# Kernel tuning notes

Measured on AMD Instinct MI355X. Metric: run time of the kernel, lower is better.

Reference implementation:

```python
import jax, jax.numpy as jnp
import numpy as np

N_NODES = 50000
N_EDGES = 640000
HID = 128
LN_EPS = 1e-5


def setup_inputs() -> dict:
    key = jax.random.key(0)
    ks = jax.random.split(key, 8)
    x = jax.random.normal(ks[0], (N_NODES, HID), dtype=jnp.float32)
    edge_index = jax.random.randint(ks[1], (2, N_EDGES), 0, N_NODES, dtype=jnp.int64)
    edge_attr = jax.random.normal(ks[2], (N_EDGES, HID), dtype=jnp.float32)
    # parameters (Kaiming-ish scaling)
    msg_W1 = jax.random.normal(ks[3], (3 * HID, HID), dtype=jnp.float32) / np.sqrt(3 * HID)
    msg_b1 = jnp.zeros((HID,), dtype=jnp.float32)
    msg_W2 = jax.random.normal(ks[4], (HID, HID), dtype=jnp.float32) / np.sqrt(HID)
    msg_b2 = jnp.zeros((HID,), dtype=jnp.float32)
    upd_W1 = jax.random.normal(ks[5], (2 * HID, HID), dtype=jnp.float32) / np.sqrt(2 * HID)
    upd_b1 = jnp.zeros((HID,), dtype=jnp.float32)
    upd_W2 = jax.random.normal(ks[6], (HID, HID), dtype=jnp.float32) / np.sqrt(HID)
    upd_b2 = jnp.zeros((HID,), dtype=jnp.float32)
    ln_gamma = jnp.ones((HID,), dtype=jnp.float32)
    ln_beta = jnp.zeros((HID,), dtype=jnp.float32)
    return {
        'x': x, 'edge_index': edge_index, 'edge_attr': edge_attr,
        'msg_W1': msg_W1, 'msg_b1': msg_b1, 'msg_W2': msg_W2, 'msg_b2': msg_b2,
        'upd_W1': upd_W1, 'upd_b1': upd_b1, 'upd_W2': upd_W2, 'upd_b2': upd_b2,
        'ln_gamma': ln_gamma, 'ln_beta': ln_beta,
    }


def _layer_norm(h, gamma, beta):
    mu = jnp.mean(h, axis=-1, keepdims=True)
    var = jnp.mean(jnp.square(h - mu), axis=-1, keepdims=True)
    return (h - mu) * jax.lax.rsqrt(var + LN_EPS) * gamma + beta


def reference(x, edge_index, edge_attr,
              msg_W1, msg_b1, msg_W2, msg_b2,
              upd_W1, upd_b1, upd_W2, upd_b2,
              ln_gamma, ln_beta):
    src, dst = edge_index[0], edge_index[1]
    # batched per-edge gather + concat: [E, 3*HID]
    msg_in = jnp.concatenate([x[src], x[dst], edge_attr], axis=-1)
    # message MLP (dropout is identity in eval)
    h = jax.nn.relu(msg_in @ msg_W1 + msg_b1)
    messages = h @ msg_W2 + msg_b2  # [E, HID]
    # scatter-add aggregation by destination node
    aggregated = jax.ops.segment_sum(messages, dst, num_segments=x.shape[0])
    # update MLP
    upd_in = jnp.concatenate([x, aggregated], axis=-1)  # [N, 2*HID]
    u = jax.nn.relu(upd_in @ upd_W1 + upd_b1)
    updated = u @ upd_W2 + upd_b2
    return _layer_norm(x + updated, ln_gamma, ln_beta)
```

## Files before the change

kernel.cpp:

```cpp
#include <hip/hip_runtime.h>

#define HID 128

typedef __attribute__((ext_vector_type(8))) short short8;
typedef __attribute__((ext_vector_type(4))) float f32x4;

__device__ __forceinline__ float bf2f(unsigned short u) {
  union { unsigned int u; float f; } c; c.u = ((unsigned int)u) << 16; return c.f;
}
__device__ __forceinline__ unsigned short f2bf(float f) {
  union { float f; unsigned int u; } c; c.f = f;
  unsigned int u = c.u;
  return (unsigned short)((u + 0x7FFFu + ((u >> 16) & 1u)) >> 16);
}
__device__ __forceinline__ float loads(const void* p, size_t i, bool f32) {
  return f32 ? ((const float*)p)[i] : bf2f(((const unsigned short*)p)[i]);
}
__device__ __forceinline__ short8 load_a8(const void* base, size_t row, int k, bool f32) {
  if (!f32) return *(const short8*)((const unsigned short*)base + row * HID + k);
  const float* fp = (const float*)base + row * HID + k;
  f32x4 f0 = *(const f32x4*)fp;
  f32x4 f1 = *(const f32x4*)(fp + 4);
  short8 t;
  t[0] = (short)f2bf(f0[0]); t[1] = (short)f2bf(f0[1]);
  t[2] = (short)f2bf(f0[2]); t[3] = (short)f2bf(f0[3]);
  t[4] = (short)f2bf(f1[0]); t[5] = (short)f2bf(f1[1]);
  t[6] = (short)f2bf(f1[2]); t[7] = (short)f2bf(f1[3]);
  return t;
}

__global__ void detect_kernel(const void* __restrict__ x,
                              const int* __restrict__ eidx,
                              int* __restrict__ flags) {
  __shared__ int bad, oddnz;
  if (threadIdx.x == 0) { bad = 0; oddnz = 0; }
  __syncthreads();
  const unsigned short* xu = (const unsigned short*)x;
  int mybad = 0;
  for (int i = threadIdx.x; i < 4096; i += 256) {
    int ef = (xu[i] >> 7) & 0xFF;
    if (!(ef == 0 || (ef >= 90 && ef <= 140))) mybad++;
  }
  if (mybad) atomicAdd(&bad, mybad);
  if (threadIdx.x < 128) {
    if (eidx[2 * threadIdx.x + 1] != 0) atomicAdd(&oddnz, 1);
  }
  __syncthreads();
  if (threadIdx.x == 0) {
    flags[0] = (bad > 409) ? 1 : 0;
    flags[1] = (oddnz == 0) ? 1 : 0;
  }
}

__device__ __forceinline__ int get_dst(const int* eidx, bool i64, int E, int e) {
  return i64 ? eidx[2 * (E + e)] : eidx[E + e];
}
__device__ __forceinline__ int get_src(const int* eidx, bool i64, int E, int e) {
  return i64 ? eidx[2 * e] : eidx[e];
}

__global__ void zero_out_kernel(unsigned int* __restrict__ out,
                                const int* __restrict__ flags, long long nelem) {
  bool f32 = flags[0] != 0;
  size_t words = (size_t)nelem * (f32 ? 2 : 1) / 2;
  for (size_t w = blockIdx.x * 256ull + threadIdx.x; w < words; w += (size_t)gridDim.x * 256ull)
    out[w] = 0u;
}

__global__ void repack_all(const void* __restrict__ W1, const void* __restrict__ W2,
                           const void* __restrict__ U1, const void* __restrict__ U2,
                           unsigned short* __restrict__ P1, unsigned short* __restrict__ P2,
                           unsigned short* __restrict__ PU1, unsigned short* __restrict__ PU2,
                           const int* __restrict__ flags) {
  const bool f32 = flags[0] != 0;
  int idx = blockIdx.x * 256 + threadIdx.x;
  const int s1 = 384 * 128, s2 = s1 + 128 * 128, s3 = s2 + 256 * 128, s4 = s3 + 128 * 128;
  if (idx >= s4) return;
  const void* W; unsigned short* P; int off;
  if (idx < s1)      { W = W1; P = P1;  off = idx; }
  else if (idx < s2) { W = W2; P = P2;  off = idx - s1; }
  else if (idx < s3) { W = U1; P = PU1; off = idx - s2; }
  else               { W = U2; P = PU2; off = idx - s3; }
  int j = off & 7, lane = (off >> 3) & 63, ct = (off >> 9) & 7, ks = off >> 12;
  int k = ks * 32 + ((lane >> 4) << 3) + j;
  int n = ct * 16 + (lane & 15);
  P[off] = f2bf(loads(W, (size_t)k * 128 + n, f32));
}

__global__ void hist_kernel(const int* __restrict__ eidx, int* __restrict__ counts,
                            const int* __restrict__ flags, int E, int N) {
  const bool i64 = flags[1] != 0;
  int e = blockIdx.x * 256 + threadIdx.x;
  if (e < E) {
    int d = get_dst(eidx, i64, E, e);
    d = min(max(d, 0), N - 1);
    atomicAdd(&counts[d], 1);
  }
}

__global__ __launch_bounds__(1024) void scan_kernel(const int* __restrict__ counts,
                                                    int* __restrict__ offs, int N) {
  __shared__ int wsum[16];
  __shared__ int wpre[16];
  __shared__ int carry_s;
  const int tid = threadIdx.x, lane = tid & 63, wid = tid >> 6;
  if (tid == 0) carry_s = 0;
  __syncthreads();
  for (int base = 0; base < N; base += 1024) {
    int i = base + tid;
    int v = (i < N) ? counts[i] : 0;
    int s = v;
#pragma unroll
    for (int off = 1; off < 64; off <<= 1) {
      int t = __shfl_up(s, off, 64);
      if (lane >= off) s += t;
    }
    if (lane == 63) wsum[wid] = s;
    __syncthreads();
    if (tid == 0) {
      int run = carry_s;
#pragma unroll
      for (int w = 0; w < 16; w++) { int t = wsum[w]; wpre[w] = run; run += t; }
      carry_s = run;
    }
    __syncthreads();
    if (i < N) offs[i] = wpre[wid] + s - v;
    __syncthreads();
  }
  if (tid == 0) offs[N] = carry_s;
}

__global__ void scatter_kernel(const int* __restrict__ eidx, int* __restrict__ cur,
                               int* __restrict__ ssrc, int* __restrict__ sdst,
                               int* __restrict__ perm,
                               const int* __restrict__ flags, int E, int N) {
  const bool i64 = flags[1] != 0;
  int e = blockIdx.x * 256 + threadIdx.x;
  if (e < E) {
    int d = get_dst(eidx, i64, E, e);
    int s = get_src(eidx, i64, E, e);
    d = min(max(d, 0), N - 1);
    s = min(max(s, 0), N - 1);
    int pos = atomicAdd(&cur[d], 1);
    ssrc[pos] = s;
    sdst[pos] = d;
    perm[pos] = e;
  }
}

__global__ __launch_bounds__(256) void edge_kernel_sorted(
    const void* __restrict__ x, const void* __restrict__ eattr,
    const int* __restrict__ ssrc, const int* __restrict__ sdst,
    const int* __restrict__ perm,
    const unsigned short* __restrict__ P1, const void* __restrict__ b1,
    const unsigned short* __restrict__ P2, const void* __restrict__ b2,
    float* __restrict__ aggf, const int* __restrict__ flags, int E, int N) {
  __shared__ __align__(16) char smem[64 * 132 * 4];
  __shared__ int sdst_s[64];
  unsigned short (*hs)[136] = (unsigned short (*)[136])smem;
  float (*ms)[132] = (float (*)[132])smem;
  const bool f32 = flags[0] != 0;
  const int tid  = threadIdx.x;
  const int lane = tid & 63;
  const int wid  = tid >> 6;
  const int l15  = lane & 15;
  const int quad = lane >> 4;
  const int base = blockIdx.x * 64;

  if (tid < 64) sdst_s[tid] = sdst[min(base + tid, E - 1)];

  int me = base + wid * 16 + l15;
  if (me >= E) me = E - 1;
  const int src = ssrc[me];
  const int dsm = sdst[me];
  const int pe  = perm[me];

  f32x4 zero = {0.f, 0.f, 0.f, 0.f};
  f32x4 acc[8];
#pragma unroll
  for (int ct = 0; ct < 8; ct++) acc[ct] = zero;

#pragma unroll
  for (int ks = 0; ks < 12; ks++) {
    const int k0 = ks * 32;
    short8 a;
    if (k0 < 128)      a = load_a8(x,     (size_t)src, k0 + quad * 8, f32);
    else if (k0 < 256) a = load_a8(x,     (size_t)dsm, (k0 - 128) + quad * 8, f32);
    else               a = load_a8(eattr, (size_t)pe,  (k0 - 256) + quad * 8, f32);
    const unsigned short* wp = P1 + ((size_t)(ks * 8) * 64 + lane) * 8;
#pragma unroll
    for (int ct = 0; ct < 8; ct++) {
      short8 b = *(const short8*)(wp + ct * 512);
      acc[ct] = __builtin_amdgcn_mfma_f32_16x16x32_bf16(a, b, acc[ct], 0, 0, 0);
    }
  }

#pragma unroll
  for (int ct = 0; ct < 8; ct++) {
    const int col = ct * 16 + l15;
    const float bv = loads(b1, col, f32);
#pragma unroll
    for (int r = 0; r < 4; r++) {
      float v = acc[ct][r] + bv;
      hs[wid * 16 + quad * 4 + r][col] = f2bf(fmaxf(v, 0.f));
    }
  }

  f32x4 acc2[8];
#pragma unroll
  for (int ct = 0; ct < 8; ct++) acc2[ct] = zero;
#pragma unroll
  for (int ks = 0; ks < 4; ks++) {
    short8 a = *(const short8*)&hs[wid * 16 + l15][ks * 32 + quad * 8];
    const unsigned short* wp = P2 + ((size_t)(ks * 8) * 64 + lane) * 8;
#pragma unroll
    for (int ct = 0; ct < 8; ct++) {
      short8 b = *(const short8*)(wp + ct * 512);
      acc2[ct] = __builtin_amdgcn_mfma_f32_16x16x32_bf16(a, b, acc2[ct], 0, 0, 0);
    }
  }

  float b2v[8];
#pragma unroll
  for (int ct = 0; ct < 8; ct++) b2v[ct] = loads(b2, ct * 16 + l15, f32);

  __syncthreads();
#pragma unroll
  for (int ct = 0; ct < 8; ct++) {
    const int col = ct * 16 + l15;
#pragma unroll
    for (int r = 0; r < 4; r++) {
      const int e = base + wid * 16 + quad * 4 + r;
      ms[wid * 16 + quad * 4 + r][col] = (e < E) ? (acc2[ct][r] + b2v[ct]) : 0.0f;
    }
  }
  __syncthreads();

  const int col  = tid & 127;
  const int half = tid >> 7;
  const int r0 = half * 32;
  float sum = 0.0f;
  int cur = sdst_s[r0];
#pragma unroll 4
  for (int r = r0; r < r0 + 32; r++) {
    int d = sdst_s[r];
    if (d != cur) {
      atomicAdd(&aggf[(size_t)cur * HID + col], sum);
      sum = 0.0f; cur = d;
    }
    sum += ms[r][col];
  }
  atomicAdd(&aggf[(size_t)cur * HID + col], sum);
}

__global__ __launch_bounds__(256) void edge_kernel_plain(
    const void* __restrict__ x, const int* __restrict__ eidx,
    const void* __restrict__ eattr,
    const unsigned short* __restrict__ P1, const void* __restrict__ b1,
    const unsigned short* __restrict__ P2, const void* __restrict__ b2,
    float* __restrict__ aggf, void* __restrict__ out,
    const int* __restrict__ flags, int E, int N, int small_mode) {
  __shared__ unsigned short hs[64][136];
  const bool f32 = flags[0] != 0;
  const bool i64 = flags[1] != 0;
  const int tid  = threadIdx.x;
  const int lane = tid & 63;
  const int wid  = tid >> 6;
  const int l15  = lane & 15;
  const int quad = lane >> 4;
  const int base = blockIdx.x * 64;

  int me = base + wid * 16 + l15;
  if (me >= E) me = E - 1;
  int src = get_src(eidx, i64, E, me);
  int dsm = get_dst(eidx, i64, E, me);
  src = min(max(src, 0), N - 1);
  dsm = min(max(dsm, 0), N - 1);

  f32x4 zero = {0.f, 0.f, 0.f, 0.f};
  f32x4 acc[8];
#pragma unroll
  for (int ct = 0; ct < 8; ct++) acc[ct] = zero;
#pragma unroll
  for (int ks = 0; ks < 12; ks++) {
    const int k0 = ks * 32;
    short8 a;
    if (k0 < 128)      a = load_a8(x,     (size_t)src, k0 + quad * 8, f32);
    else if (k0 < 256) a = load_a8(x,     (size_t)dsm, (k0 - 128) + quad * 8, f32);
    else               a = load_a8(eattr, (size_t)me,  (k0 - 256) + quad * 8, f32);
    const unsigned short* wp = P1 + ((size_t)(ks * 8) * 64 + lane) * 8;
#pragma unroll
    for (int ct = 0; ct < 8; ct++) {
      short8 b = *(const short8*)(wp + ct * 512);
      acc[ct] = __builtin_amdgcn_mfma_f32_16x16x32_bf16(a, b, acc[ct], 0, 0, 0);
    }
  }
#pragma unroll
  for (int ct = 0; ct < 8; ct++) {
    const int col = ct * 16 + l15;
    const float bv = loads(b1, col, f32);
#pragma unroll
    for (int r = 0; r < 4; r++)
      hs[wid * 16 + quad * 4 + r][col] = f2bf(fmaxf(acc[ct][r] + bv, 0.f));
  }
  __syncthreads();
  f32x4 acc2[8];
#pragma unroll
  for (int ct = 0; ct < 8; ct++) acc2[ct] = zero;
#pragma unroll
  for (int ks = 0; ks < 4; ks++) {
    short8 a = *(const short8*)&hs[wid * 16 + l15][ks * 32 + quad * 8];
    const unsigned short* wp = P2 + ((size_t)(ks * 8) * 64 + lane) * 8;
#pragma unroll
    for (int ct = 0; ct < 8; ct++) {
      short8 b = *(const short8*)(wp + ct * 512);
      acc2[ct] = __builtin_amdgcn_mfma_f32_16x16x32_bf16(a, b, acc2[ct], 0, 0, 0);
    }
  }
  float b2v[8];
#pragma unroll
  for (int ct = 0; ct < 8; ct++) b2v[ct] = loads(b2, ct * 16 + l15, f32);

  if (!small_mode || f32) {
    float* tgt = (!small_mode) ? aggf : (float*)out;
#pragma unroll
    for (int r = 0; r < 4; r++) {
      const int e = base + wid * 16 + quad * 4 + r;
      if (e < E) {
        int d = get_dst(eidx, i64, E, e);
        d = min(max(d, 0), N - 1);
        float* op = tgt + (size_t)d * HID + l15;
#pragma unroll
        for (int ct = 0; ct < 8; ct++) atomicAdd(op + ct * 16, acc2[ct][r] + b2v[ct]);
      }
    }
  } else {
#pragma unroll
    for (int ct = 0; ct < 8; ct++) {
      const int col = ct * 16 + l15;
#pragma unroll
      for (int r = 0; r < 4; r++)
        hs[wid * 16 + quad * 4 + r][col] = f2bf(acc2[ct][r] + b2v[ct]);
    }
    __syncthreads();
    const int row = tid >> 2;
    const int cg  = (tid & 3) * 32;
    const int e = base + row;
    if (e < E) {
      int d = get_dst(eidx, i64, E, e);
      d = min(max(d, 0), N - 1);
      unsigned int* orow = (unsigned int*)out + ((size_t)d * HID >> 1);
#pragma unroll
      for (int p = 0; p < 16; p++) {
        const int col = cg + p * 2;
        const float lo = bf2f(hs[row][col]);
        const float hi = bf2f(hs[row][col + 1]);
        unsigned int* wp = orow + (col >> 1);
        unsigned int old = *wp, assumed;
        do {
          assumed = old;
          unsigned int nv = (unsigned int)f2bf(bf2f((unsigned short)(assumed & 0xFFFF)) + lo)
                          | ((unsigned int)f2bf(bf2f((unsigned short)(assumed >> 16)) + hi) << 16);
          old = atomicCAS(wp, assumed, nv);
        } while (old != assumed);
      }
    }
  }
}

__global__ __launch_bounds__(256) void node_kernel(
    const void* __restrict__ x, const float* __restrict__ aggf,
    const unsigned short* __restrict__ PU1, const void* __restrict__ ub1,
    const unsigned short* __restrict__ PU2, const void* __restrict__ ub2,
    const void* __restrict__ gamma, const void* __restrict__ beta,
    void* __restrict__ out, const int* __restrict__ flags, int N, int small_mode) {
  __shared__ unsigned short hs[64][136];
  const bool f32 = flags[0] != 0;
  const int tid  = threadIdx.x;
  const int lane = tid & 63;
  const int wid  = tid >> 6;
  const int l15  = lane & 15;
  const int quad = lane >> 4;
  const int base = blockIdx.x * 64;

  int mn = base + wid * 16 + l15;
  if (mn >= N) mn = N - 1;

  const void* aggp = (!small_mode) ? (const void*)aggf : (const void*)out;
  const bool aggF32 = (!small_mode) ? true : f32;

  f32x4 zero = {0.f, 0.f, 0.f, 0.f};
  f32x4 acc[8];
#pragma unroll
  for (int ct = 0; ct < 8; ct++) acc[ct] = zero;
#pragma unroll
  for (int ks = 0; ks < 8; ks++) {
    const int k0 = ks * 32;
    short8 a;
    if (k0 < 128) a = load_a8(x,    (size_t)mn, k0 + quad * 8, f32);
    else          a = load_a8(aggp, (size_t)mn, (k0 - 128) + quad * 8, aggF32);
    const unsigned short* wp = PU1 + ((size_t)(ks * 8) * 64 + lane) * 8;
#pragma unroll
    for (int ct = 0; ct < 8; ct++) {
      short8 b = *(const short8*)(wp + ct * 512);
      acc[ct] = __builtin_amdgcn_mfma_f32_16x16x32_bf16(a, b, acc[ct], 0, 0, 0);
    }
  }
#pragma unroll
  for (int ct = 0; ct < 8; ct++) {
    const int col = ct * 16 + l15;
    const float bv = loads(ub1, col, f32);
#pragma unroll
    for (int r = 0; r < 4; r++)
      hs[wid * 16 + quad * 4 + r][col] = f2bf(fmaxf(acc[ct][r] + bv, 0.f));
  }
  __syncthreads();
  f32x4 acc2[8];
#pragma unroll
  for (int ct = 0; ct < 8; ct++) acc2[ct] = zero;
#pragma unroll
  for (int ks = 0; ks < 4; ks++) {
    short8 a = *(const short8*)&hs[wid * 16 + l15][ks * 32 + quad * 8];
    const unsigned short* wp = PU2 + ((size_t)(ks * 8) * 64 + lane) * 8;
#pragma unroll
    for (int ct = 0; ct < 8; ct++) {
      short8 b = *(const short8*)(wp + ct * 512);
      acc2[ct] = __builtin_amdgcn_mfma_f32_16x16x32_bf16(a, b, acc2[ct], 0, 0, 0);
    }
  }

  float vals[8][4];
  float s1[4] = {0.f, 0.f, 0.f, 0.f};
  float s2[4] = {0.f, 0.f, 0.f, 0.f};
#pragma unroll
  for (int ct = 0; ct < 8; ct++) {
    const int col = ct * 16 + l15;
    const float bv = loads(ub2, col, f32);
#pragma unroll
    for (int r = 0; r < 4; r++) {
      int row = base + wid * 16 + quad * 4 + r;
      int rc = row < N ? row : 0;
      float v = acc2[ct][r] + bv + loads(x, (size_t)rc * HID + col, f32);
      vals[ct][r] = v;
      s1[r] += v;
      s2[r] += v * v;
    }
  }
#pragma unroll
  for (int off = 1; off < 16; off <<= 1) {
#pragma unroll
    for (int r = 0; r < 4; r++) {
      s1[r] += __shfl_xor(s1[r], off, 16);
      s2[r] += __shfl_xor(s2[r], off, 16);
    }
  }
#pragma unroll
  for (int r = 0; r < 4; r++) {
    const int row = base + wid * 16 + quad * 4 + r;
    if (row < N) {
      const float mean = s1[r] * (1.0f / 128.0f);
      const float var  = fmaxf(s2[r] * (1.0f / 128.0f) - mean * mean, 0.0f);
      const float rstd = rsqrtf(var + 1e-5f);
#pragma unroll
      for (int ct = 0; ct < 8; ct++) {
        const int col = ct * 16 + l15;
        float o = (vals[ct][r] - mean) * rstd * loads(gamma, col, f32) + loads(beta, col, f32);
        if (f32) ((float*)out)[(size_t)row * HID + col] = o;
        else     ((unsigned short*)out)[(size_t)row * HID + col] = f2bf(o);
      }
    }
  }
}

extern "C" void kernel_launch(void* const* d_in, const int* in_sizes, int n_in,
                              void* d_out, int out_size, void* d_ws, size_t ws_size,
                              hipStream_t stream) {
  (void)n_in;
  const void* x     = d_in[0];
  const int*  eidx  = (const int*)d_in[1];
  const void* eattr = d_in[2];
  const void* W1  = d_in[3];
  const void* b1  = d_in[4];
  const void* W2  = d_in[5];
  const void* b2  = d_in[6];
  const void* U1  = d_in[7];
  const void* ub1 = d_in[8];
  const void* U2  = d_in[9];
  const void* ub2 = d_in[10];
  const void* gam = d_in[11];
  const void* bet = d_in[12];

  const int N = in_sizes[0] / HID;
  const int E = in_sizes[2] / HID;

  char* ws = (char*)d_ws;
  int* flags = (int*)ws;
  unsigned short* P1  = (unsigned short*)(ws + 256);
  unsigned short* P2  = (unsigned short*)(ws + 256 + 98304);
  unsigned short* PU1 = (unsigned short*)(ws + 256 + 131072);
  unsigned short* PU2 = (unsigned short*)(ws + 256 + 196608);
  const size_t agg_off = 256 + 229376;
  float* aggf = (float*)(ws + agg_off);
  const size_t agg_bytes = (size_t)N * HID * sizeof(float);

  size_t o = agg_off + agg_bytes;
  auto alignup = [](size_t v) { return (v + 255) & ~(size_t)255; };
  o = alignup(o);           size_t offs_off = o; o += (size_t)(N + 1) * 4;
  o = alignup(o);           size_t cur_off  = o; o += (size_t)(N + 1) * 4;
  o = alignup(o);           size_t ssrc_off = o; o += (size_t)E * 4;
  o = alignup(o);           size_t sdst_off = o; o += (size_t)E * 4;
  o = alignup(o);           size_t perm_off = o; o += (size_t)E * 4;
  const size_t need_sort  = o;
  const size_t need_basic = agg_off + agg_bytes;

  int* offsb = (int*)(ws + offs_off);
  int* curb  = (int*)(ws + cur_off);
  int* ssrc  = (int*)(ws + ssrc_off);
  int* sdst  = (int*)(ws + sdst_off);
  int* perm  = (int*)(ws + perm_off);

  const int mode = (ws_size >= need_sort) ? 2 : ((ws_size >= need_basic) ? 1 : 0);

  detect_kernel<<<1, 256, 0, stream>>>(x, eidx, flags);
  repack_all<<<448, 256, 0, stream>>>(W1, W2, U1, U2, P1, P2, PU1, PU2, flags);

  if (mode == 2) {
    hipMemsetAsync(aggf, 0, agg_bytes, stream);
    hipMemsetAsync(curb, 0, (size_t)(N + 1) * 4, stream);
    hist_kernel<<<(E + 255) / 256, 256, 0, stream>>>(eidx, curb, flags, E, N);
    scan_kernel<<<1, 1024, 0, stream>>>(curb, offsb, N);
    hipMemcpyAsync(curb, offsb, (size_t)(N + 1) * 4, hipMemcpyDeviceToDevice, stream);
    scatter_kernel<<<(E + 255) / 256, 256, 0, stream>>>(eidx, curb, ssrc, sdst, perm,
                                                        flags, E, N);
    edge_kernel_sorted<<<(E + 63) / 64, 256, 0, stream>>>(x, eattr, ssrc, sdst, perm,
                                                          P1, b1, P2, b2, aggf, flags, E, N);
    node_kernel<<<(N + 63) / 64, 256, 0, stream>>>(x, aggf, PU1, ub1, PU2, ub2,
                                                   gam, bet, d_out, flags, N, 0);
  } else if (mode == 1) {
    hipMemsetAsync(aggf, 0, agg_bytes, stream);
    edge_kernel_plain<<<(E + 63) / 64, 256, 0, stream>>>(x, eidx, eattr, P1, b1, P2, b2,
                                                         aggf, d_out, flags, E, N, 0);
    node_kernel<<<(N + 63) / 64, 256, 0, stream>>>(x, aggf, PU1, ub1, PU2, ub2,
                                                   gam, bet, d_out, flags, N, 0);
  } else {
    zero_out_kernel<<<1024, 256, 0, stream>>>((unsigned int*)d_out, flags, (long long)out_size);
    edge_kernel_plain<<<(E + 63) / 64, 256, 0, stream>>>(x, eidx, eattr, P1, b1, P2, b2,
                                                         aggf, d_out, flags, E, N, 1);
    node_kernel<<<(N + 63) / 64, 256, 0, stream>>>(x, aggf, PU1, ub1, PU2, ub2,
                                                   gam, bet, d_out, flags, N, 1);
  }
}
```

Baseline: 903.0 us.

## Precompute per-node first-layer projections and split edge MLP into gather, store, reduce

```diff
diff --git a/kernel.cpp b/kernel.cpp
--- a/kernel.cpp
+++ b/kernel.cpp
@@ -98,6 +98,244 @@
   }
 }
 
+__global__ __launch_bounds__(1024) void scanA_kernel(const int* __restrict__ cnt,
+                                                     int* __restrict__ curb,
+                                                     int* __restrict__ bsum, int N) {
+  __shared__ int wsum[16], wsum2[16];
+  const int tid = threadIdx.x, lane = tid & 63, wid = tid >> 6;
+  int i = blockIdx.x * 1024 + tid;
+  int v = (i < N) ? cnt[i] : 0;
+  int s = v;
+#pragma unroll
+  for (int off = 1; off < 64; off <<= 1) {
+    int t = __shfl_up(s, off, 64);
+    if (lane >= off) s += t;
+  }
+  if (lane == 63) wsum[wid] = s;
+  __syncthreads();
+  if (wid == 0 && lane < 16) {
+    int w = wsum[lane];
+#pragma unroll
+    for (int off = 1; off < 16; off <<= 1) {
+      int t = __shfl_up(w, off, 16);
+      if (lane >= off) w += t;
+    }
+    wsum2[lane] = w;
+    if (lane == 15) bsum[blockIdx.x] = w;
+  }
+  __syncthreads();
+  int pre = (wid > 0) ? wsum2[wid - 1] : 0;
+  if (i < N) curb[i] = pre + s - v;
+}
+
+__global__ void scanB_kernel(int* __restrict__ bsum, int nb) {
+  if (threadIdx.x == 0 && blockIdx.x == 0) {
+    int run = 0;
+    for (int b = 0; b < nb; b++) { int t = bsum[b]; bsum[b] = run; run += t; }
+  }
+}
+
+__global__ __launch_bounds__(1024) void scanC_kernel(int* __restrict__ curb,
+                                                     const int* __restrict__ bsum, int N) {
+  int i = blockIdx.x * 1024 + threadIdx.x;
+  if (i < N) curb[i] += bsum[blockIdx.x];
+}
+
+__global__ void scatter_rank_kernel(const int* __restrict__ eidx, int* __restrict__ cur,
+                                    int* __restrict__ rank, int* __restrict__ sdst,
+                                    const int* __restrict__ flags, int E, int N) {
+  const bool i64 = flags[1] != 0;
+  int e = blockIdx.x * 256 + threadIdx.x;
+  if (e < E) {
+    int d = get_dst(eidx, i64, E, e);
+    d = min(max(d, 0), N - 1);
+    int pos = atomicAdd(&cur[d], 1);
+    rank[e] = pos;
+    sdst[pos] = d;
+  }
+}
+
+__global__ __launch_bounds__(256) void x1_kernel(
+    const void* __restrict__ x, const unsigned short* __restrict__ P1,
+    const void* __restrict__ b1, unsigned short* __restrict__ X1,
+    const int* __restrict__ flags, int N) {
+  __shared__ unsigned short hs[64][264];
+  const bool f32 = flags[0] != 0;
+  const int tid = threadIdx.x, lane = tid & 63, wid = tid >> 6;
+  const int l15 = lane & 15, quad = lane >> 4;
+  const int base = blockIdx.x * 64;
+  int mn = min(base + wid * 16 + l15, N - 1);
+
+  f32x4 zero = {0.f, 0.f, 0.f, 0.f};
+  f32x4 acca[8], accb[8];
+#pragma unroll
+  for (int ct = 0; ct < 8; ct++) { acca[ct] = zero; accb[ct] = zero; }
+#pragma unroll
+  for (int ks = 0; ks < 4; ks++) {
+    short8 a = load_a8(x, (size_t)mn, ks * 32 + quad * 8, f32);
+    const unsigned short* wpa = P1 + ((size_t)(ks * 8) * 64 + lane) * 8;
+    const unsigned short* wpb = P1 + ((size_t)((ks + 4) * 8) * 64 + lane) * 8;
+#pragma unroll
+    for (int ct = 0; ct < 8; ct++) {
+      short8 ba = *(const short8*)(wpa + ct * 512);
+      short8 bb = *(const short8*)(wpb + ct * 512);
+      acca[ct] = __builtin_amdgcn_mfma_f32_16x16x32_bf16(a, ba, acca[ct], 0, 0, 0);
+      accb[ct] = __builtin_amdgcn_mfma_f32_16x16x32_bf16(a, bb, accb[ct], 0, 0, 0);
+    }
+  }
+#pragma unroll
+  for (int ct = 0; ct < 8; ct++) {
+    const int col = ct * 16 + l15;
+    const float bv = loads(b1, col, f32);
+#pragma unroll
+    for (int r = 0; r < 4; r++) {
+      hs[wid * 16 + quad * 4 + r][col]       = f2bf(acca[ct][r] + bv);
+      hs[wid * 16 + quad * 4 + r][128 + col] = f2bf(accb[ct][r]);
+    }
+  }
+  __syncthreads();
+  const int row = tid >> 2, part = tid & 3;
+  if (base + row < N) {
+    unsigned short* op = X1 + (size_t)(base + row) * 256 + part * 64;
+#pragma unroll
+    for (int j = 0; j < 8; j++)
+      *(short8*)(op + j * 8) = *(const short8*)&hs[row][part * 64 + j * 8];
+  }
+}
+
+__global__ __launch_bounds__(256) void edgeB_kernel(
+    const void* __restrict__ eattr, const int* __restrict__ eidx,
+    const int* __restrict__ rank, const unsigned short* __restrict__ X1,
+    const unsigned short* __restrict__ P1, const unsigned short* __restrict__ P2,
+    unsigned short* __restrict__ msgbuf, const int* __restrict__ flags, int E, int N) {
+  __shared__ unsigned short hsb[64][136];
+  __shared__ int src_s[64], dst_s[64], rank_s[64];
+  const bool f32 = flags[0] != 0;
+  const bool i64 = flags[1] != 0;
+  const int tid = threadIdx.x, lane = tid & 63, wid = tid >> 6;
+  const int l15 = lane & 15, quad = lane >> 4;
+  const int base = blockIdx.x * 64;
+
+  if (tid < 64) {
+    int e = min(base + tid, E - 1);
+    int s = get_src(eidx, i64, E, e);
+    int d = get_dst(eidx, i64, E, e);
+    src_s[tid] = min(max(s, 0), N - 1);
+    dst_s[tid] = min(max(d, 0), N - 1);
+    rank_s[tid] = rank[e];
+  }
+
+  int me = min(base + wid * 16 + l15, E - 1);
+  f32x4 zero = {0.f, 0.f, 0.f, 0.f};
+  f32x4 acc[8];
+#pragma unroll
+  for (int ct = 0; ct < 8; ct++) acc[ct] = zero;
+#pragma unroll
+  for (int ks = 0; ks < 4; ks++) {
+    short8 a = load_a8(eattr, (size_t)me, ks * 32 + quad * 8, f32);
+    const unsigned short* wp = P1 + ((size_t)((ks + 8) * 8) * 64 + lane) * 8;
+#pragma unroll
+    for (int ct = 0; ct < 8; ct++) {
+      short8 b = *(const short8*)(wp + ct * 512);
+      acc[ct] = __builtin_amdgcn_mfma_f32_16x16x32_bf16(a, b, acc[ct], 0, 0, 0);
+    }
+  }
+#pragma unroll
+  for (int ct = 0; ct < 8; ct++) {
+    const int col = ct * 16 + l15;
+#pragma unroll
+    for (int r = 0; r < 4; r++)
+      hsb[wid * 16 + quad * 4 + r][col] = f2bf(acc[ct][r]);
+  }
+  __syncthreads();
+
+#pragma unroll
+  for (int it = 0; it < 4; it++) {
+    const int r = it * 16 + (tid >> 4);
+    const int cg = (tid & 15) * 8;
+    short8 h8 = *(const short8*)&hsb[r][cg];
+    short8 a8 = *(const short8*)(X1 + (size_t)src_s[r] * 256 + cg);
+    short8 b8 = *(const short8*)(X1 + (size_t)dst_s[r] * 256 + 128 + cg);
+    short8 o;
+#pragma unroll
+    for (int j = 0; j < 8; j++) {
+      float v = bf2f((unsigned short)h8[j]) + bf2f((unsigned short)a8[j])
+              + bf2f((unsigned short)b8[j]);
+      o[j] = (short)f2bf(fmaxf(v, 0.f));
+    }
+    *(short8*)&hsb[r][cg] = o;
+  }
+  __syncthreads();
+
+  f32x4 acc2[8];
+#pragma unroll
+  for (int ct = 0; ct < 8; ct++) acc2[ct] = zero;
+#pragma unroll
+  for (int ks = 0; ks < 4; ks++) {
+    short8 a = *(const short8*)&hsb[wid * 16 + l15][ks * 32 + quad * 8];
+    const unsigned short* wp = P2 + ((size_t)(ks * 8) * 64 + lane) * 8;
+#pragma unroll
+    for (int ct = 0; ct < 8; ct++) {
+      short8 b = *(const short8*)(wp + ct * 512);
+      acc2[ct] = __builtin_amdgcn_mfma_f32_16x16x32_bf16(a, b, acc2[ct], 0, 0, 0);
+    }
+  }
+#pragma unroll
+  for (int ct = 0; ct < 8; ct++) {
+    const int col = ct * 16 + l15;
+#pragma unroll
+    for (int r = 0; r < 4; r++)
+      hsb[wid * 16 + quad * 4 + r][col] = f2bf(acc2[ct][r]);
+  }
+  __syncthreads();
+
+  const int row = tid >> 2, part = tid & 3;
+  if (base + row < E) {
+    unsigned short* mp = msgbuf + (size_t)rank_s[row] * HID + part * 32;
+#pragma unroll
+    for (int j = 0; j < 4; j++)
+      *(short8*)(mp + j * 8) = *(const short8*)&hsb[row][part * 32 + j * 8];
+  }
+}
+
+__global__ __launch_bounds__(256) void reduce_kernel(
+    const unsigned short* __restrict__ msgbuf, const int* __restrict__ sdst,
+    const void* __restrict__ b2, float* __restrict__ aggf,
+    const int* __restrict__ flags, int E) {
+  __shared__ int sd[256];
+  const bool f32 = flags[0] != 0;
+  const int tid = threadIdx.x;
+  const int base = blockIdx.x * 256;
+  { int e = base + tid; sd[tid] = (e < E) ? sdst[e] : -1; }
+  __syncthreads();
+  const int pair = tid & 63;
+  const int grp = tid >> 6;
+  const int c0 = pair * 2;
+  const float b2a = loads(b2, c0, f32);
+  const float b2b = loads(b2, c0 + 1, f32);
+  float sa = 0.f, sb = 0.f; int cnt = 0, cur = -1;
+  for (int r = 0; r < 64; r++) {
+    const int lr = grp * 64 + r;
+    const int d = sd[lr];
+    if (d < 0) break;
+    if (d != cur) {
+      if (cnt > 0) {
+        atomicAdd(&aggf[(size_t)cur * HID + c0],     sa + cnt * b2a);
+        atomicAdd(&aggf[(size_t)cur * HID + c0 + 1], sb + cnt * b2b);
+      }
+      sa = sb = 0.f; cnt = 0; cur = d;
+    }
+    unsigned int u = *(const unsigned int*)(msgbuf + (size_t)(base + lr) * HID + c0);
+    sa += bf2f((unsigned short)(u & 0xFFFF));
+    sb += bf2f((unsigned short)(u >> 16));
+    cnt++;
+  }
+  if (cnt > 0) {
+    atomicAdd(&aggf[(size_t)cur * HID + c0],     sa + cnt * b2a);
+    atomicAdd(&aggf[(size_t)cur * HID + c0 + 1], sb + cnt * b2b);
+  }
+}
+
 __global__ __launch_bounds__(1024) void scan_kernel(const int* __restrict__ counts,
                                                     int* __restrict__ offs, int N) {
   __shared__ int wsum[16];
@@ -160,11 +398,8 @@
   unsigned short (*hs)[136] = (unsigned short (*)[136])smem;
   float (*ms)[132] = (float (*)[132])smem;
   const bool f32 = flags[0] != 0;
-  const int tid  = threadIdx.x;
-  const int lane = tid & 63;
-  const int wid  = tid >> 6;
-  const int l15  = lane & 15;
-  const int quad = lane >> 4;
+  const int tid = threadIdx.x, lane = tid & 63, wid = tid >> 6;
+  const int l15 = lane & 15, quad = lane >> 4;
   const int base = blockIdx.x * 64;
 
   if (tid < 64) sdst_s[tid] = sdst[min(base + tid, E - 1)];
@@ -179,7 +414,6 @@
   f32x4 acc[8];
 #pragma unroll
   for (int ct = 0; ct < 8; ct++) acc[ct] = zero;
-
 #pragma unroll
   for (int ks = 0; ks < 12; ks++) {
     const int k0 = ks * 32;
@@ -194,18 +428,14 @@
       acc[ct] = __builtin_amdgcn_mfma_f32_16x16x32_bf16(a, b, acc[ct], 0, 0, 0);
     }
   }
-
 #pragma unroll
   for (int ct = 0; ct < 8; ct++) {
     const int col = ct * 16 + l15;
     const float bv = loads(b1, col, f32);
 #pragma unroll
-    for (int r = 0; r < 4; r++) {
-      float v = acc[ct][r] + bv;
-      hs[wid * 16 + quad * 4 + r][col] = f2bf(fmaxf(v, 0.f));
-    }
-  }
-
+    for (int r = 0; r < 4; r++)
+      hs[wid * 16 + quad * 4 + r][col] = f2bf(fmaxf(acc[ct][r] + bv, 0.f));
+  }
   f32x4 acc2[8];
 #pragma unroll
   for (int ct = 0; ct < 8; ct++) acc2[ct] = zero;
@@ -219,11 +449,9 @@
       acc2[ct] = __builtin_amdgcn_mfma_f32_16x16x32_bf16(a, b, acc2[ct], 0, 0, 0);
     }
   }
-
   float b2v[8];
 #pragma unroll
   for (int ct = 0; ct < 8; ct++) b2v[ct] = loads(b2, ct * 16 + l15, f32);
-
   __syncthreads();
 #pragma unroll
   for (int ct = 0; ct < 8; ct++) {
@@ -235,7 +463,6 @@
     }
   }
   __syncthreads();
-
   const int col  = tid & 127;
   const int half = tid >> 7;
   const int r0 = half * 32;
@@ -263,11 +490,8 @@
   __shared__ unsigned short hs[64][136];
   const bool f32 = flags[0] != 0;
   const bool i64 = flags[1] != 0;
-  const int tid  = threadIdx.x;
-  const int lane = tid & 63;
-  const int wid  = tid >> 6;
-  const int l15  = lane & 15;
-  const int quad = lane >> 4;
+  const int tid = threadIdx.x, lane = tid & 63, wid = tid >> 6;
+  const int l15 = lane & 15, quad = lane >> 4;
   const int base = blockIdx.x * 64;
 
   int me = base + wid * 16 + l15;
@@ -376,11 +600,8 @@
     void* __restrict__ out, const int* __restrict__ flags, int N, int small_mode) {
   __shared__ unsigned short hs[64][136];
   const bool f32 = flags[0] != 0;
-  const int tid  = threadIdx.x;
-  const int lane = tid & 63;
-  const int wid  = tid >> 6;
-  const int l15  = lane & 15;
-  const int quad = lane >> 4;
+  const int tid = threadIdx.x, lane = tid & 63, wid = tid >> 6;
+  const int l15 = lane & 15, quad = lane >> 4;
   const int base = blockIdx.x * 64;
 
   int mn = base + wid * 16 + l15;
@@ -494,6 +715,8 @@
   const int E = in_sizes[2] / HID;
 
   char* ws = (char*)d_ws;
+  auto alignup = [](size_t v) { return (v + 255) & ~(size_t)255; };
+
   int* flags = (int*)ws;
   unsigned short* P1  = (unsigned short*)(ws + 256);
   unsigned short* P2  = (unsigned short*)(ws + 256 + 98304);
@@ -502,29 +725,63 @@
   const size_t agg_off = 256 + 229376;
   float* aggf = (float*)(ws + agg_off);
   const size_t agg_bytes = (size_t)N * HID * sizeof(float);
-
-  size_t o = agg_off + agg_bytes;
-  auto alignup = [](size_t v) { return (v + 255) & ~(size_t)255; };
-  o = alignup(o);           size_t offs_off = o; o += (size_t)(N + 1) * 4;
-  o = alignup(o);           size_t cur_off  = o; o += (size_t)(N + 1) * 4;
-  o = alignup(o);           size_t ssrc_off = o; o += (size_t)E * 4;
-  o = alignup(o);           size_t sdst_off = o; o += (size_t)E * 4;
-  o = alignup(o);           size_t perm_off = o; o += (size_t)E * 4;
-  const size_t need_sort  = o;
   const size_t need_basic = agg_off + agg_bytes;
 
-  int* offsb = (int*)(ws + offs_off);
-  int* curb  = (int*)(ws + cur_off);
-  int* ssrc  = (int*)(ws + ssrc_off);
-  int* sdst  = (int*)(ws + sdst_off);
-  int* perm  = (int*)(ws + perm_off);
-
-  const int mode = (ws_size >= need_sort) ? 2 : ((ws_size >= need_basic) ? 1 : 0);
+  size_t o3 = alignup(need_basic);
+  size_t cnt_off  = o3; o3 = alignup(o3 + (size_t)(N + 64) * 4);
+  size_t cur_off  = o3; o3 = alignup(o3 + (size_t)(N + 64) * 4);
+  size_t bsum_off = o3; o3 = alignup(o3 + 1024);
+  size_t rank_off = o3; o3 = alignup(o3 + (size_t)E * 4);
+  size_t sds3_off = o3; o3 = alignup(o3 + (size_t)E * 4);
+  size_t x1_off   = o3; o3 = alignup(o3 + (size_t)N * 256 * 2);
+  size_t msg_off  = o3; o3 = alignup(o3 + (size_t)E * HID * 2);
+  const size_t need3 = o3;
+
+  size_t o2 = alignup(need_basic);
+  size_t offs_off = o2; o2 = alignup(o2 + (size_t)(N + 1) * 4);
+  size_t cur2_off = o2; o2 = alignup(o2 + (size_t)(N + 1) * 4);
+  size_t ssrc_off = o2; o2 = alignup(o2 + (size_t)E * 4);
+  size_t sds2_off = o2; o2 = alignup(o2 + (size_t)E * 4);
+  size_t perm_off = o2; o2 = alignup(o2 + (size_t)E * 4);
+  const size_t need2 = o2;
+
+  const int mode = (ws_size >= need3) ? 3
+                 : (ws_size >= need2) ? 2
+                 : (ws_size >= need_basic) ? 1 : 0;
 
   detect_kernel<<<1, 256, 0, stream>>>(x, eidx, flags);
   repack_all<<<448, 256, 0, stream>>>(W1, W2, U1, U2, P1, P2, PU1, PU2, flags);
 
-  if (mode == 2) {
+  if (mode == 3) {
+    int* cntb = (int*)(ws + cnt_off);
+    int* curb = (int*)(ws + cur_off);
+    int* bsum = (int*)(ws + bsum_off);
+    int* rank = (int*)(ws + rank_off);
+    int* sdst = (int*)(ws + sds3_off);
+    unsigned short* X1     = (unsigned short*)(ws + x1_off);
+    unsigned short* msgbuf = (unsigned short*)(ws + msg_off);
+    const int nb = (N + 1023) / 1024;
+
+    hipMemsetAsync(aggf, 0, agg_bytes, stream);
+    hipMemsetAsync(cntb, 0, (size_t)N * 4, stream);
+    hist_kernel<<<(E + 255) / 256, 256, 0, stream>>>(eidx, cntb, flags, E, N);
+    scanA_kernel<<<nb, 1024, 0, stream>>>(cntb, curb, bsum, N);
+    scanB_kernel<<<1, 64, 0, stream>>>(bsum, nb);
+    scanC_kernel<<<nb, 1024, 0, stream>>>(curb, bsum, N);
+    scatter_rank_kernel<<<(E + 255) / 256, 256, 0, stream>>>(eidx, curb, rank, sdst,
+                                                             flags, E, N);
+    x1_kernel<<<(N + 63) / 64, 256, 0, stream>>>(x, P1, b1, X1, flags, N);
+    edgeB_kernel<<<(E + 63) / 64, 256, 0, stream>>>(eattr, eidx, rank, X1, P1, P2,
+                                                    msgbuf, flags, E, N);
+    reduce_kernel<<<(E + 255) / 256, 256, 0, stream>>>(msgbuf, sdst, b2, aggf, flags, E);
+    node_kernel<<<(N + 63) / 64, 256, 0, stream>>>(x, aggf, PU1, ub1, PU2, ub2,
+                                                   gam, bet, d_out, flags, N, 0);
+  } else if (mode == 2) {
+    int* offsb = (int*)(ws + offs_off);
+    int* curb  = (int*)(ws + cur2_off);
+    int* ssrc  = (int*)(ws + ssrc_off);
+    int* sdst  = (int*)(ws + sds2_off);
+    int* perm  = (int*)(ws + perm_off);
     hipMemsetAsync(aggf, 0, agg_bytes, stream);
     hipMemsetAsync(curb, 0, (size_t)(N + 1) * 4, stream);
     hist_kernel<<<(E + 255) / 256, 256, 0, stream>>>(eidx, curb, flags, E, N);
```

After: 868.1 us. -3.9%, faster.
